# Kernel optimization log

Hardware: AMD Instinct MI355X
Metric: run time of the kernel (lower is better)

## Reference

```python
import jax, jax.numpy as jnp
import numpy as np

SAMPLE_RATE = 48000.0
B, T, F = 32, 48000, 5


def setup_inputs() -> dict:
    key = jax.random.key(0)
    k1, k2, k3 = jax.random.split(key, 3)
    excitation = jax.random.normal(k1, (B, T, 1), dtype=jnp.float32)
    # realistic formant center frequencies (200..4000 Hz) and bandwidths (50..400 Hz)
    cf = 200.0 + 3800.0 * jax.random.uniform(k2, (B, T, F), dtype=jnp.float32)
    bw = 50.0 + 350.0 * jax.random.uniform(k3, (B, T, F), dtype=jnp.float32)
    states = jnp.zeros((B, F, 2), dtype=jnp.float32)
    return {"excitation": excitation, "cf": cf, "bw": bw, "states": states}


def _formant_filter(excitation, cf, bw, states):
    # biquad coefficients from pole radius r and angle theta, per (b, t, f)
    r = jnp.exp(-jnp.pi * bw / SAMPLE_RATE)
    theta = (2.0 * jnp.pi) * cf / SAMPLE_RATE
    a1 = -2.0 * r * jnp.cos(theta)            # [B,T,F]
    a2 = r * r                                 # [B,T,F]
    gain = (1.0 - r * r) * jnp.sin(theta)      # [B,T,F]
    x = excitation * gain                      # broadcast [B,T,1]*[B,T,F] -> [B,T,F]

    y1 = states[:, :, 0]                       # [B,F]
    y2 = states[:, :, 1]                       # [B,F]

    def step(carry, inp):
        y1, y2 = carry
        xt, a1t, a2t = inp                     # each [B,F]
        yt = xt - a1t * y1 - a2t * y2
        return (yt, y1), yt

    # time-major for scan
    xs = (jnp.swapaxes(x, 0, 1), jnp.swapaxes(a1, 0, 1), jnp.swapaxes(a2, 0, 1))
    (y1, y2), ys = jax.lax.scan(step, (y1, y2), xs)   # ys: [T,B,F]

    out = jnp.swapaxes(ys, 0, 1).sum(axis=-1, keepdims=True)  # [B,T,1]
    new_states = jnp.stack([y1, y2], axis=2)                   # [B,F,2]
    return out, new_states


def reference(excitation, cf, bw, states):
    return _formant_filter(excitation, cf, bw, states)
```

## Files before the change

kernel.cpp:

```cpp
#include <hip/hip_runtime.h>


constexpr int B = 32;
constexpr int T = 48000;
constexpr int F = 5;
constexpr int L = 16;
constexpr int C = T / L;
constexpr int GS = 64;
constexpr int NG = (C + GS - 1) / GS;
constexpr int NCHAIN = B * F;
constexpr int THREADS = GS * F;
constexpr int MSTRIDE = 7;
constexpr int MROW = GS * MSTRIDE;

#define CBW2 (-9.4416635e-05f)
#define CCF  (1.3089969e-04f)

__device__ __forceinline__ float fast_exp2(float x) {
#if __has_builtin(__builtin_amdgcn_exp2f)
  return __builtin_amdgcn_exp2f(x);
#else
  return exp2f(x);
#endif
}

__device__ __forceinline__ void chunk_map(
    const float* __restrict__ exc, const float* __restrict__ cf,
    const float* __restrict__ bw, int b, int c, int f,
    float& u1, float& u2, float& v1, float& v2, float& w1, float& w2) {
  int t0 = c * L;
  const float* cfp = cf + (size_t)(b * T + t0) * F + f;
  const float* bwp = bw + (size_t)(b * T + t0) * F + f;
  const float* ep  = exc + (size_t)b * T + t0;
  #pragma unroll
  for (int i = 0; i < L; ++i) {
    float bwf = bwp[(size_t)i * F];
    float cff = cfp[(size_t)i * F];
    float e   = ep[i];
    float r  = fast_exp2(CBW2 * bwf);
    float th = CCF * cff;
    float sn = __sinf(th);
    float cs = __cosf(th);
    float p = 2.f * r * cs;
    float q = -r * r;
    float g = fmaf(q, sn, sn);
    float x = e * g;
    float nu = fmaf(p, u1, q * u2);
    float nv = fmaf(p, v1, q * v2);
    float nw = fmaf(p, w1, fmaf(q, w2, x));
    u2 = u1; u1 = nu;
    v2 = v1; v1 = nv;
    w2 = w1; w1 = nw;
  }
}

__device__ __forceinline__ void wave_scan_maps(int lane, float& u1, float& u2,
                                               float& v1, float& v2,
                                               float& w1, float& w2) {
  #pragma unroll
  for (int d = 1; d < 64; d <<= 1) {
    float pu1 = __shfl_up(u1, d);
    float pv1 = __shfl_up(v1, d);
    float pu2 = __shfl_up(u2, d);
    float pv2 = __shfl_up(v2, d);
    float pw1 = __shfl_up(w1, d);
    float pw2 = __shfl_up(w2, d);
    bool has = (lane >= d);
    pu1 = has ? pu1 : 1.f;  pv1 = has ? pv1 : 0.f;
    pu2 = has ? pu2 : 0.f;  pv2 = has ? pv2 : 1.f;
    pw1 = has ? pw1 : 0.f;  pw2 = has ? pw2 : 0.f;
    float nu1 = fmaf(u1, pu1, v1 * pu2);
    float nv1 = fmaf(u1, pv1, v1 * pv2);
    float nu2 = fmaf(u2, pu1, v2 * pu2);
    float nv2 = fmaf(u2, pv1, v2 * pv2);
    float nw1 = fmaf(u1, pw1, fmaf(v1, pw2, w1));
    float nw2 = fmaf(u2, pw1, fmaf(v2, pw2, w2));
    u1 = nu1; v1 = nv1; u2 = nu2; v2 = nv2; w1 = nw1; w2 = nw2;
  }
}

__global__ __launch_bounds__(THREADS) void k1_kernel(
    const float* __restrict__ exc, const float* __restrict__ cf,
    const float* __restrict__ bw, float* __restrict__ Aws,
    float* __restrict__ Gprod) {
  __shared__ float smaps[F][MROW];

  int bg = blockIdx.x;
  int b = bg / NG;
  int g = bg % NG;
  int tid = threadIdx.x;
  int c_local = tid / F;
  int f = tid % F;
  int c = g * GS + c_local;

  float u1 = 1.f, u2 = 0.f, v1 = 0.f, v2 = 1.f, w1 = 0.f, w2 = 0.f;
  if (c < C) chunk_map(exc, cf, bw, b, c, f, u1, u2, v1, v2, w1, w2);

  float* m = &smaps[f][c_local * MSTRIDE];
  m[0] = u1; m[1] = u2; m[2] = v1; m[3] = v2; m[4] = w1; m[5] = w2;
  __syncthreads();

  int w = tid >> 6;
  int lane = tid & 63;
  const float* s = &smaps[w][lane * MSTRIDE];
  float a1 = s[0], a2 = s[1], a3 = s[2], a4 = s[3], a5 = s[4], a6 = s[5];
  wave_scan_maps(lane, a1, a2, a3, a4, a5, a6);

  int c2 = g * GS + lane;
  int chain = b * F + w;
  if (c2 < C) {
    float4* o = (float4*)(Aws + ((size_t)chain * C + c2) * 8);
    o[0] = make_float4(a1, a2, a3, a4);
    o[1] = make_float4(a5, a6, 0.f, 0.f);
  }
  if (lane == 63) {
    float4* gp = (float4*)(Gprod + (size_t)(chain * NG + g) * 8);
    gp[0] = make_float4(a1, a2, a3, a4);
    gp[1] = make_float4(a5, a6, 0.f, 0.f);
  }
}

__global__ __launch_bounds__(64) void k2_kernel(
    const float* __restrict__ Gprod, const float* __restrict__ states0,
    float* __restrict__ Sg, float* __restrict__ out_states) {
  int chain = blockIdx.x;
  int lane = threadIdx.x;

  float u1 = 1.f, u2 = 0.f, v1 = 0.f, v2 = 1.f, w1 = 0.f, w2 = 0.f;
  if (lane < NG) {
    const float4* gp = (const float4*)(Gprod + (size_t)(chain * NG + lane) * 8);
    float4 A0 = gp[0];
    float4 A1 = gp[1];
    u1 = A0.x; u2 = A0.y; v1 = A0.z; v2 = A0.w; w1 = A1.x; w2 = A1.y;
  }

  wave_scan_maps(lane, u1, u2, v1, v2, w1, w2);

  float s01 = states0[chain * 2 + 0];
  float s02 = states0[chain * 2 + 1];

  float eu1 = __shfl_up(u1, 1), ev1 = __shfl_up(v1, 1);
  float eu2 = __shfl_up(u2, 1), ev2 = __shfl_up(v2, 1);
  float ew1 = __shfl_up(w1, 1), ew2 = __shfl_up(w2, 1);
  if (lane == 0) { eu1 = 1.f; ev1 = 0.f; eu2 = 0.f; ev2 = 1.f; ew1 = 0.f; ew2 = 0.f; }
  if (lane < NG) {
    float sy1 = fmaf(eu1, s01, fmaf(ev1, s02, ew1));
    float sy2 = fmaf(eu2, s01, fmaf(ev2, s02, ew2));
    *(float2*)(Sg + (size_t)(chain * NG + lane) * 2) = make_float2(sy1, sy2);
  }

  float ay1 = fmaf(u1, s01, fmaf(v1, s02, w1));
  float ay2 = fmaf(u2, s01, fmaf(v2, s02, w2));
  float fy1 = __shfl(ay1, 63);
  float fy2 = __shfl(ay2, 63);
  if (lane == 0) {
    out_states[chain * 2 + 0] = fy1;
    out_states[chain * 2 + 1] = fy2;
  }
}

constexpr int P3_ROW = GS * (L + 1);

__global__ __launch_bounds__(THREADS) void k3_kernel(
    const float* __restrict__ exc, const float* __restrict__ cf,
    const float* __restrict__ bw, const float* __restrict__ Aws,
    const float* __restrict__ Sg, float* __restrict__ out) {
  __shared__ float red[F][P3_ROW];

  int bg = blockIdx.x;
  int b = bg / NG;
  int g = bg % NG;
  int c0 = g * GS;
  int nc = (C - c0 < GS) ? (C - c0) : GS;

  int tid = threadIdx.x;
  int c_local = tid / F;
  int f = tid % F;

  if (c_local < nc) {
    int c = c0 + c_local;
    int chain = b * F + f;

    float2 sg = *(const float2*)(Sg + (size_t)(chain * NG + g) * 2);
    float y1, y2;
    if (c_local == 0) {
      y1 = sg.x;
      y2 = sg.y;
    } else {
      const float4* m = (const float4*)(Aws + ((size_t)chain * C + (c - 1)) * 8);
      float4 M0 = m[0];
      float4 M1 = m[1];
      y1 = fmaf(M0.x, sg.x, fmaf(M0.z, sg.y, M1.x));
      y2 = fmaf(M0.y, sg.x, fmaf(M0.w, sg.y, M1.y));
    }

    int t0 = c * L;
    const float* cfp = cf + (size_t)(b * T + t0) * F + f;
    const float* bwp = bw + (size_t)(b * T + t0) * F + f;
    const float* ep  = exc + (size_t)b * T + t0;

    #pragma unroll
    for (int i = 0; i < L; ++i) {
      float bwf = bwp[(size_t)i * F];
      float cff = cfp[(size_t)i * F];
      float e   = ep[i];
      float r  = fast_exp2(CBW2 * bwf);
      float th = CCF * cff;
      float sn = __sinf(th);
      float cs = __cosf(th);
      float p = 2.f * r * cs;
      float q = -r * r;
      float gn = fmaf(q, sn, sn);
      float x = e * gn;
      float y = fmaf(p, y1, fmaf(q, y2, x));
      red[f][c_local * (L + 1) + i] = y;
      y2 = y1;
      y1 = y;
    }
  }

  __syncthreads();

  int nt = nc * L;
  int tbase = b * T + c0 * L;
  for (int t = tid; t < nt; t += THREADS) {
    int ci = t >> 4;
    int ii = t & (L - 1);
    int a = ci * (L + 1) + ii;
    float s = red[0][a] + red[1][a] + red[2][a] + red[3][a] + red[4][a];
    out[tbase + t] = s;
  }
}

extern "C" void kernel_launch(void* const* d_in, const int* in_sizes, int n_in,
                              void* d_out, int out_size, void* d_ws, size_t ws_size,
                              hipStream_t stream) {
  const float* exc = (const float*)d_in[0];
  const float* cf  = (const float*)d_in[1];
  const float* bw  = (const float*)d_in[2];
  const float* st  = (const float*)d_in[3];
  float* out        = (float*)d_out;
  float* out_states = out + (size_t)B * T;

  float* Aws   = (float*)d_ws;
  float* Gprod = Aws + (size_t)NCHAIN * C * 8;
  float* Sg    = Gprod + (size_t)NCHAIN * NG * 8;

  k1_kernel<<<B * NG, THREADS, 0, stream>>>(exc, cf, bw, Aws, Gprod);
  k2_kernel<<<NCHAIN, 64, 0, stream>>>(Gprod, st, Sg, out_states);
  k3_kernel<<<B * NG, THREADS, 0, stream>>>(exc, cf, bw, Aws, Sg, out);
}
```

Before: 44.63 us.

## Stage cf/bw/excitation tiles in shared memory with coalesced float4 loads

Both the chunk-map kernel and the final filtering kernel now cooperatively load each block's cf, bw and excitation tile into padded shared memory using coalesced float4 reads, rather than each thread reading strided elements (stride F) from global memory. K3 also reuses the staged cf buffer in place to hold filter outputs for the reduction over formants. The goal is better global memory coalescing. In exchange, shared memory use per block grows (about 46KB), which may reduce occupancy, and extra barriers are added.

Measured after the change: 55.09 us. 23.4% more time.

```diff
diff --git a/kernel.cpp b/kernel.cpp
--- a/kernel.cpp
+++ b/kernel.cpp
@@ -13,6 +13,9 @@
 constexpr int MSTRIDE = 7;
 constexpr int MROW = GS * MSTRIDE;
 
+constexpr int CF_STRIDE = L * F + 4;
+constexpr int EX_STRIDE = L + 4;
+
 #define CBW2 (-9.4416635e-05f)
 #define CCF  (1.3089969e-04f)
 
@@ -24,33 +27,32 @@
 #endif
 }
 
-__device__ __forceinline__ void chunk_map(
-    const float* __restrict__ exc, const float* __restrict__ cf,
-    const float* __restrict__ bw, int b, int c, int f,
-    float& u1, float& u2, float& v1, float& v2, float& w1, float& w2) {
-  int t0 = c * L;
-  const float* cfp = cf + (size_t)(b * T + t0) * F + f;
-  const float* bwp = bw + (size_t)(b * T + t0) * F + f;
-  const float* ep  = exc + (size_t)b * T + t0;
-  #pragma unroll
-  for (int i = 0; i < L; ++i) {
-    float bwf = bwp[(size_t)i * F];
-    float cff = cfp[(size_t)i * F];
-    float e   = ep[i];
-    float r  = fast_exp2(CBW2 * bwf);
-    float th = CCF * cff;
-    float sn = __sinf(th);
-    float cs = __cosf(th);
-    float p = 2.f * r * cs;
-    float q = -r * r;
-    float g = fmaf(q, sn, sn);
-    float x = e * g;
-    float nu = fmaf(p, u1, q * u2);
-    float nv = fmaf(p, v1, q * v2);
-    float nw = fmaf(p, w1, fmaf(q, w2, x));
-    u2 = u1; u1 = nu;
-    v2 = v1; v1 = nv;
-    w2 = w1; w1 = nw;
+struct Stage {
+  float cf[GS * CF_STRIDE];
+  float bw[GS * CF_STRIDE];
+  float ex[GS * EX_STRIDE];
+};
+
+__device__ __forceinline__ void stage_inputs(
+    Stage& st, const float* __restrict__ exc, const float* __restrict__ cf,
+    const float* __restrict__ bw, int b, int g, int nc, int tid) {
+  size_t t0 = (size_t)g * (GS * L);
+  const float4* csrc = (const float4*)(cf + ((size_t)b * T + t0) * F);
+  const float4* bsrc = (const float4*)(bw + ((size_t)b * T + t0) * F);
+  const float4* esrc = (const float4*)(exc + (size_t)b * T + t0);
+  int nvec = nc * 20;
+  for (int k = tid; k < nvec; k += THREADS) {
+    float4 v = csrc[k];
+    *(float4*)&st.cf[(k / 20) * CF_STRIDE + (k % 20) * 4] = v;
+  }
+  for (int k = tid; k < nvec; k += THREADS) {
+    float4 v = bsrc[k];
+    *(float4*)&st.bw[(k / 20) * CF_STRIDE + (k % 20) * 4] = v;
+  }
+  int nve = nc * 4;
+  for (int k = tid; k < nve; k += THREADS) {
+    float4 v = esrc[k];
+    *(float4*)&st.ex[(k / 4) * EX_STRIDE + (k % 4) * 4] = v;
   }
 }
 
@@ -79,34 +81,70 @@
   }
 }
 
+union SharedK1 {
+  Stage st;
+  float smaps[F][MROW];
+};
+
 __global__ __launch_bounds__(THREADS) void k1_kernel(
     const float* __restrict__ exc, const float* __restrict__ cf,
     const float* __restrict__ bw, float* __restrict__ Aws,
     float* __restrict__ Gprod) {
-  __shared__ float smaps[F][MROW];
+  __shared__ SharedK1 sh;
 
   int bg = blockIdx.x;
   int b = bg / NG;
   int g = bg % NG;
+  int c0 = g * GS;
+  int nc = (C - c0 < GS) ? (C - c0) : GS;
   int tid = threadIdx.x;
   int c_local = tid / F;
   int f = tid % F;
-  int c = g * GS + c_local;
+
+  stage_inputs(sh.st, exc, cf, bw, b, g, nc, tid);
+  __syncthreads();
 
   float u1 = 1.f, u2 = 0.f, v1 = 0.f, v2 = 1.f, w1 = 0.f, w2 = 0.f;
-  if (c < C) chunk_map(exc, cf, bw, b, c, f, u1, u2, v1, v2, w1, w2);
-
-  float* m = &smaps[f][c_local * MSTRIDE];
-  m[0] = u1; m[1] = u2; m[2] = v1; m[3] = v2; m[4] = w1; m[5] = w2;
+  if (c_local < nc) {
+    const float* cfp = &sh.st.cf[c_local * CF_STRIDE + f];
+    const float* bwp = &sh.st.bw[c_local * CF_STRIDE + f];
+    const float* ep  = &sh.st.ex[c_local * EX_STRIDE];
+    #pragma unroll
+    for (int i = 0; i < L; ++i) {
+      float bwf = bwp[i * F];
+      float cff = cfp[i * F];
+      float e   = ep[i];
+      float r  = fast_exp2(CBW2 * bwf);
+      float th = CCF * cff;
+      float sn = __sinf(th);
+      float cs = __cosf(th);
+      float p = 2.f * r * cs;
+      float q = -r * r;
+      float gn = fmaf(q, sn, sn);
+      float x = e * gn;
+      float nu = fmaf(p, u1, q * u2);
+      float nv = fmaf(p, v1, q * v2);
+      float nw = fmaf(p, w1, fmaf(q, w2, x));
+      u2 = u1; u1 = nu;
+      v2 = v1; v1 = nv;
+      w2 = w1; w1 = nw;
+    }
+  }
+  __syncthreads();
+
+  {
+    float* m = &sh.smaps[f][c_local * MSTRIDE];
+    m[0] = u1; m[1] = u2; m[2] = v1; m[3] = v2; m[4] = w1; m[5] = w2;
+  }
   __syncthreads();
 
   int w = tid >> 6;
   int lane = tid & 63;
-  const float* s = &smaps[w][lane * MSTRIDE];
+  const float* s = &sh.smaps[w][lane * MSTRIDE];
   float a1 = s[0], a2 = s[1], a3 = s[2], a4 = s[3], a5 = s[4], a6 = s[5];
   wave_scan_maps(lane, a1, a2, a3, a4, a5, a6);
 
-  int c2 = g * GS + lane;
+  int c2 = c0 + lane;
   int chain = b * F + w;
   if (c2 < C) {
     float4* o = (float4*)(Aws + ((size_t)chain * C + c2) * 8);
@@ -159,23 +197,23 @@
   }
 }
 
-constexpr int P3_ROW = GS * (L + 1);
-
 __global__ __launch_bounds__(THREADS) void k3_kernel(
     const float* __restrict__ exc, const float* __restrict__ cf,
     const float* __restrict__ bw, const float* __restrict__ Aws,
     const float* __restrict__ Sg, float* __restrict__ out) {
-  __shared__ float red[F][P3_ROW];
+  __shared__ Stage st;
 
   int bg = blockIdx.x;
   int b = bg / NG;
   int g = bg % NG;
   int c0 = g * GS;
   int nc = (C - c0 < GS) ? (C - c0) : GS;
-
   int tid = threadIdx.x;
   int c_local = tid / F;
   int f = tid % F;
+
+  stage_inputs(st, exc, cf, bw, b, g, nc, tid);
+  __syncthreads();
 
   if (c_local < nc) {
     int c = c0 + c_local;
@@ -194,15 +232,14 @@
       y2 = fmaf(M0.y, sg.x, fmaf(M0.w, sg.y, M1.y));
     }
 
-    int t0 = c * L;
-    const float* cfp = cf + (size_t)(b * T + t0) * F + f;
-    const float* bwp = bw + (size_t)(b * T + t0) * F + f;
-    const float* ep  = exc + (size_t)b * T + t0;
+    float* cfp = &st.cf[c_local * CF_STRIDE + f];
+    const float* bwp = &st.bw[c_local * CF_STRIDE + f];
+    const float* ep  = &st.ex[c_local * EX_STRIDE];
 
     #pragma unroll
     for (int i = 0; i < L; ++i) {
-      float bwf = bwp[(size_t)i * F];
-      float cff = cfp[(size_t)i * F];
+      float bwf = bwp[i * F];
+      float cff = cfp[i * F];
       float e   = ep[i];
       float r  = fast_exp2(CBW2 * bwf);
       float th = CCF * cff;
@@ -213,21 +250,18 @@
       float gn = fmaf(q, sn, sn);
       float x = e * gn;
       float y = fmaf(p, y1, fmaf(q, y2, x));
-      red[f][c_local * (L + 1) + i] = y;
+      cfp[i * F] = y;
       y2 = y1;
       y1 = y;
     }
   }
-
   __syncthreads();
 
   int nt = nc * L;
-  int tbase = b * T + c0 * L;
+  size_t tbase = (size_t)b * T + (size_t)c0 * L;
   for (int t = tid; t < nt; t += THREADS) {
-    int ci = t >> 4;
-    int ii = t & (L - 1);
-    int a = ci * (L + 1) + ii;
-    float s = red[0][a] + red[1][a] + red[2][a] + red[3][a] + red[4][a];
+    const float* yrow = &st.cf[(t >> 4) * CF_STRIDE + (t & (L - 1)) * F];
+    float s = yrow[0] + yrow[1] + yrow[2] + yrow[3] + yrow[4];
     out[tbase + t] = s;
   }
 }
```

## Fold group-level carry scan into output kernel and prefetch chunk inputs

Applied to the files above, without the earlier changes.

Removes the separate carry-scan kernel: every block of the final kernel now re-scans its chain's group products with a wave scan and picks the prefix it needs, writing final states from group 0. This saves one launch and the round trip through global memory for the seed states. In exchange each block repeats a small redundant scan. It also software-prefetches the coefficient and excitation inputs in tiles of four with a vectorised excitation load, and pads the shared arrays by one element to shift bank mapping.

After: 43.05 us. 1.04x faster.

```diff
diff --git a/kernel.cpp b/kernel.cpp
--- a/kernel.cpp
+++ b/kernel.cpp
@@ -10,8 +10,10 @@
 constexpr int NG = (C + GS - 1) / GS;
 constexpr int NCHAIN = B * F;
 constexpr int THREADS = GS * F;
+constexpr int NBG = B * NG;
 constexpr int MSTRIDE = 7;
-constexpr int MROW = GS * MSTRIDE;
+constexpr int MROW = GS * MSTRIDE + 1;
+constexpr int RROW = GS * (L + 1) + 1;
 
 #define CBW2 (-9.4416635e-05f)
 #define CCF  (1.3089969e-04f)
@@ -24,34 +26,15 @@
 #endif
 }
 
-__device__ __forceinline__ void chunk_map(
-    const float* __restrict__ exc, const float* __restrict__ cf,
-    const float* __restrict__ bw, int b, int c, int f,
-    float& u1, float& u2, float& v1, float& v2, float& w1, float& w2) {
-  int t0 = c * L;
-  const float* cfp = cf + (size_t)(b * T + t0) * F + f;
-  const float* bwp = bw + (size_t)(b * T + t0) * F + f;
-  const float* ep  = exc + (size_t)b * T + t0;
-  #pragma unroll
-  for (int i = 0; i < L; ++i) {
-    float bwf = bwp[(size_t)i * F];
-    float cff = cfp[(size_t)i * F];
-    float e   = ep[i];
-    float r  = fast_exp2(CBW2 * bwf);
-    float th = CCF * cff;
-    float sn = __sinf(th);
-    float cs = __cosf(th);
-    float p = 2.f * r * cs;
-    float q = -r * r;
-    float g = fmaf(q, sn, sn);
-    float x = e * g;
-    float nu = fmaf(p, u1, q * u2);
-    float nv = fmaf(p, v1, q * v2);
-    float nw = fmaf(p, w1, fmaf(q, w2, x));
-    u2 = u1; u1 = nu;
-    v2 = v1; v1 = nv;
-    w2 = w1; w1 = nw;
-  }
+__device__ __forceinline__ void coef(float cff, float bwf, float e,
+                                     float& p, float& q, float& x) {
+  float r  = fast_exp2(CBW2 * bwf);
+  float th = CCF * cff;
+  float sn = __sinf(th);
+  float cs = __cosf(th);
+  p = 2.f * r * cs;
+  q = -r * r;
+  x = e * fmaf(q, sn, sn);
 }
 
 __device__ __forceinline__ void wave_scan_maps(int lane, float& u1, float& u2,
@@ -86,22 +69,60 @@
   __shared__ float smaps[F][MROW];
 
   int bg = blockIdx.x;
-  int b = bg / NG;
-  int g = bg % NG;
+  int b = bg / NG, g = bg % NG;
   int tid = threadIdx.x;
-  int c_local = tid / F;
-  int f = tid % F;
+  int c_local = tid / F, f = tid % F;
   int c = g * GS + c_local;
 
   float u1 = 1.f, u2 = 0.f, v1 = 0.f, v2 = 1.f, w1 = 0.f, w2 = 0.f;
-  if (c < C) chunk_map(exc, cf, bw, b, c, f, u1, u2, v1, v2, w1, w2);
-
-  float* m = &smaps[f][c_local * MSTRIDE];
-  m[0] = u1; m[1] = u2; m[2] = v1; m[3] = v2; m[4] = w1; m[5] = w2;
+  if (c < C) {
+    const float* cfp = cf + ((size_t)b * T + c * L) * F + f;
+    const float* bwp = bw + ((size_t)b * T + c * L) * F + f;
+    const float4* ep4 = (const float4*)(exc + (size_t)b * T + c * L);
+
+    float4 e = ep4[0];
+    float cfa[4], bwa[4];
+    #pragma unroll
+    for (int j = 0; j < 4; ++j) { cfa[j] = cfp[j * F]; bwa[j] = bwp[j * F]; }
+
+    #pragma unroll
+    for (int tile = 0; tile < 4; ++tile) {
+      float4 en;
+      float cfn[4], bwn[4];
+      if (tile < 3) {
+        en = ep4[tile + 1];
+        #pragma unroll
+        for (int j = 0; j < 4; ++j) {
+          cfn[j] = cfp[(tile * 4 + 4 + j) * F];
+          bwn[j] = bwp[(tile * 4 + 4 + j) * F];
+        }
+      }
+      #pragma unroll
+      for (int j = 0; j < 4; ++j) {
+        float p, q, x;
+        coef(cfa[j], bwa[j], (&e.x)[j], p, q, x);
+        float nu = fmaf(p, u1, q * u2);
+        float nv = fmaf(p, v1, q * v2);
+        float nw = fmaf(p, w1, fmaf(q, w2, x));
+        u2 = u1; u1 = nu;
+        v2 = v1; v1 = nv;
+        w2 = w1; w1 = nw;
+      }
+      if (tile < 3) {
+        e = en;
+        #pragma unroll
+        for (int j = 0; j < 4; ++j) { cfa[j] = cfn[j]; bwa[j] = bwn[j]; }
+      }
+    }
+  }
+
+  {
+    float* m = &smaps[f][c_local * MSTRIDE];
+    m[0] = u1; m[1] = u2; m[2] = v1; m[3] = v2; m[4] = w1; m[5] = w2;
+  }
   __syncthreads();
 
-  int w = tid >> 6;
-  int lane = tid & 63;
+  int w = tid >> 6, lane = tid & 63;
   const float* s = &smaps[w][lane * MSTRIDE];
   float a1 = s[0], a2 = s[1], a3 = s[2], a4 = s[3], a5 = s[4], a6 = s[5];
   wave_scan_maps(lane, a1, a2, a3, a4, a5, a6);
@@ -120,72 +141,57 @@
   }
 }
 
-__global__ __launch_bounds__(64) void k2_kernel(
-    const float* __restrict__ Gprod, const float* __restrict__ states0,
-    float* __restrict__ Sg, float* __restrict__ out_states) {
-  int chain = blockIdx.x;
-  int lane = threadIdx.x;
-
-  float u1 = 1.f, u2 = 0.f, v1 = 0.f, v2 = 1.f, w1 = 0.f, w2 = 0.f;
-  if (lane < NG) {
-    const float4* gp = (const float4*)(Gprod + (size_t)(chain * NG + lane) * 8);
-    float4 A0 = gp[0];
-    float4 A1 = gp[1];
-    u1 = A0.x; u2 = A0.y; v1 = A0.z; v2 = A0.w; w1 = A1.x; w2 = A1.y;
-  }
-
-  wave_scan_maps(lane, u1, u2, v1, v2, w1, w2);
-
-  float s01 = states0[chain * 2 + 0];
-  float s02 = states0[chain * 2 + 1];
-
-  float eu1 = __shfl_up(u1, 1), ev1 = __shfl_up(v1, 1);
-  float eu2 = __shfl_up(u2, 1), ev2 = __shfl_up(v2, 1);
-  float ew1 = __shfl_up(w1, 1), ew2 = __shfl_up(w2, 1);
-  if (lane == 0) { eu1 = 1.f; ev1 = 0.f; eu2 = 0.f; ev2 = 1.f; ew1 = 0.f; ew2 = 0.f; }
-  if (lane < NG) {
-    float sy1 = fmaf(eu1, s01, fmaf(ev1, s02, ew1));
-    float sy2 = fmaf(eu2, s01, fmaf(ev2, s02, ew2));
-    *(float2*)(Sg + (size_t)(chain * NG + lane) * 2) = make_float2(sy1, sy2);
-  }
-
-  float ay1 = fmaf(u1, s01, fmaf(v1, s02, w1));
-  float ay2 = fmaf(u2, s01, fmaf(v2, s02, w2));
-  float fy1 = __shfl(ay1, 63);
-  float fy2 = __shfl(ay2, 63);
-  if (lane == 0) {
-    out_states[chain * 2 + 0] = fy1;
-    out_states[chain * 2 + 1] = fy2;
-  }
-}
-
-constexpr int P3_ROW = GS * (L + 1);
-
 __global__ __launch_bounds__(THREADS) void k3_kernel(
     const float* __restrict__ exc, const float* __restrict__ cf,
     const float* __restrict__ bw, const float* __restrict__ Aws,
-    const float* __restrict__ Sg, float* __restrict__ out) {
-  __shared__ float red[F][P3_ROW];
+    const float* __restrict__ Gprod, const float* __restrict__ states0,
+    float* __restrict__ out, float* __restrict__ out_states) {
+  __shared__ float red[F][RROW];
+  __shared__ float2 sgb[F];
 
   int bg = blockIdx.x;
-  int b = bg / NG;
-  int g = bg % NG;
+  int b = bg / NG, g = bg % NG;
   int c0 = g * GS;
   int nc = (C - c0 < GS) ? (C - c0) : GS;
-
   int tid = threadIdx.x;
-  int c_local = tid / F;
-  int f = tid % F;
+  int c_local = tid / F, f = tid % F;
+  int w = tid >> 6, lane = tid & 63;
+
+  {
+    int chain = b * F + w;
+    float u1 = 1.f, u2 = 0.f, v1 = 0.f, v2 = 1.f, w1 = 0.f, w2 = 0.f;
+    if (lane < NG) {
+      const float4* gp = (const float4*)(Gprod + (size_t)(chain * NG + lane) * 8);
+      float4 A0 = gp[0];
+      float4 A1 = gp[1];
+      u1 = A0.x; u2 = A0.y; v1 = A0.z; v2 = A0.w; w1 = A1.x; w2 = A1.y;
+    }
+    wave_scan_maps(lane, u1, u2, v1, v2, w1, w2);
+
+    float s01 = states0[chain * 2 + 0];
+    float s02 = states0[chain * 2 + 1];
+    if (g == 0) {
+      if (lane == 0) sgb[w] = make_float2(s01, s02);
+      if (lane == NG - 1) {
+        out_states[chain * 2 + 0] = fmaf(u1, s01, fmaf(v1, s02, w1));
+        out_states[chain * 2 + 1] = fmaf(u2, s01, fmaf(v2, s02, w2));
+      }
+    } else if (lane == g - 1) {
+      float sy1 = fmaf(u1, s01, fmaf(v1, s02, w1));
+      float sy2 = fmaf(u2, s01, fmaf(v2, s02, w2));
+      sgb[w] = make_float2(sy1, sy2);
+    }
+  }
+  __syncthreads();
 
   if (c_local < nc) {
     int c = c0 + c_local;
     int chain = b * F + f;
 
-    float2 sg = *(const float2*)(Sg + (size_t)(chain * NG + g) * 2);
+    float2 sg = sgb[f];
     float y1, y2;
     if (c_local == 0) {
-      y1 = sg.x;
-      y2 = sg.y;
+      y1 = sg.x; y2 = sg.y;
     } else {
       const float4* m = (const float4*)(Aws + ((size_t)chain * C + (c - 1)) * 8);
       float4 M0 = m[0];
@@ -194,39 +200,50 @@
       y2 = fmaf(M0.y, sg.x, fmaf(M0.w, sg.y, M1.y));
     }
 
-    int t0 = c * L;
-    const float* cfp = cf + (size_t)(b * T + t0) * F + f;
-    const float* bwp = bw + (size_t)(b * T + t0) * F + f;
-    const float* ep  = exc + (size_t)b * T + t0;
-
-    #pragma unroll
-    for (int i = 0; i < L; ++i) {
-      float bwf = bwp[(size_t)i * F];
-      float cff = cfp[(size_t)i * F];
-      float e   = ep[i];
-      float r  = fast_exp2(CBW2 * bwf);
-      float th = CCF * cff;
-      float sn = __sinf(th);
-      float cs = __cosf(th);
-      float p = 2.f * r * cs;
-      float q = -r * r;
-      float gn = fmaf(q, sn, sn);
-      float x = e * gn;
-      float y = fmaf(p, y1, fmaf(q, y2, x));
-      red[f][c_local * (L + 1) + i] = y;
-      y2 = y1;
-      y1 = y;
-    }
-  }
-
+    const float* cfp = cf + ((size_t)b * T + c * L) * F + f;
+    const float* bwp = bw + ((size_t)b * T + c * L) * F + f;
+    const float4* ep4 = (const float4*)(exc + (size_t)b * T + c * L);
+
+    float4 e = ep4[0];
+    float cfa[4], bwa[4];
+    #pragma unroll
+    for (int j = 0; j < 4; ++j) { cfa[j] = cfp[j * F]; bwa[j] = bwp[j * F]; }
+
+    float* rrow = &red[f][c_local * (L + 1)];
+    #pragma unroll
+    for (int tile = 0; tile < 4; ++tile) {
+      float4 en;
+      float cfn[4], bwn[4];
+      if (tile < 3) {
+        en = ep4[tile + 1];
+        #pragma unroll
+        for (int j = 0; j < 4; ++j) {
+          cfn[j] = cfp[(tile * 4 + 4 + j) * F];
+          bwn[j] = bwp[(tile * 4 + 4 + j) * F];
+        }
+      }
+      #pragma unroll
+      for (int j = 0; j < 4; ++j) {
+        float p, q, x;
+        coef(cfa[j], bwa[j], (&e.x)[j], p, q, x);
+        float y = fmaf(p, y1, fmaf(q, y2, x));
+        rrow[tile * 4 + j] = y;
+        y2 = y1;
+        y1 = y;
+      }
+      if (tile < 3) {
+        e = en;
+        #pragma unroll
+        for (int j = 0; j < 4; ++j) { cfa[j] = cfn[j]; bwa[j] = bwn[j]; }
+      }
+    }
+  }
   __syncthreads();
 
   int nt = nc * L;
-  int tbase = b * T + c0 * L;
+  size_t tbase = (size_t)b * T + (size_t)c0 * L;
   for (int t = tid; t < nt; t += THREADS) {
-    int ci = t >> 4;
-    int ii = t & (L - 1);
-    int a = ci * (L + 1) + ii;
+    int a = (t >> 4) * (L + 1) + (t & (L - 1));
     float s = red[0][a] + red[1][a] + red[2][a] + red[3][a] + red[4][a];
     out[tbase + t] = s;
   }
@@ -244,9 +261,8 @@
 
   float* Aws   = (float*)d_ws;
   float* Gprod = Aws + (size_t)NCHAIN * C * 8;
-  float* Sg    = Gprod + (size_t)NCHAIN * NG * 8;
-
-  k1_kernel<<<B * NG, THREADS, 0, stream>>>(exc, cf, bw, Aws, Gprod);
-  k2_kernel<<<NCHAIN, 64, 0, stream>>>(Gprod, st, Sg, out_states);
-  k3_kernel<<<B * NG, THREADS, 0, stream>>>(exc, cf, bw, Aws, Sg, out);
-}
+
+  k1_kernel<<<NBG, THREADS, 0, stream>>>(exc, cf, bw, Aws, Gprod);
+  k3_kernel<<<NBG, THREADS, 0, stream>>>(exc, cf, bw, Aws, Gprod, st, out,
+                                         out_states);
+}
```
